# Optimization experiments

Measured on AMD Instinct MI355X. Metric: run time of the kernel, lower is better.

The kernel has to match this reference:

```python
import jax, jax.numpy as jnp
import numpy as np

B, H, W, C = 8, 128, 128, 192
G, K = 6, 3
K2 = K * K
GC = C // G
OFFSET_SCALE = 0.1
DN = ('NHWC', 'HWIO', 'NHWC')


def setup_inputs() -> dict:
    key = jax.random.key(0)
    ks = jax.random.split(key, 8)
    s = 1.0 / np.sqrt(C)
    return {
        'x': jax.random.normal(ks[0], (B, H, W, C), jnp.float32),
        'w_in': jax.random.normal(ks[1], (C, C), jnp.float32) * s,
        'b_in': jnp.zeros((C,), jnp.float32),
        'w_dw': jax.random.normal(ks[2], (3, 3, 1, C), jnp.float32) / 3.0,  # depthwise 3x3, HWIO
        'b_dw': jnp.zeros((C,), jnp.float32),
        'w_pw': jax.random.normal(ks[3], (1, 1, C, C), jnp.float32) * s,  # 1x1 conv
        'b_pw': jnp.zeros((C,), jnp.float32),
        'w_off': jax.random.normal(ks[4], (C, G * K2 * 2), jnp.float32) * 0.01,
        'b_off': jnp.zeros((G * K2 * 2,), jnp.float32),
        'w_mask': jax.random.normal(ks[5], (C, G * K2), jnp.float32) * 0.01,
        'b_mask': jnp.zeros((G * K2,), jnp.float32),
        'w_out': jax.random.normal(ks[6], (C, C), jnp.float32) * s,
        'b_out': jnp.zeros((C,), jnp.float32),
    }


def _deform_forward(x, w_in, b_in, w_dw, b_dw, w_pw, b_pw, w_off, b_off, w_mask, b_mask, w_out, b_out):
    x_proj = x @ w_in + b_in  # [B,H,W,C]

    # dw_conv: depthwise 3x3 -> SiLU -> 1x1 pointwise (all channels-last)
    xd = jax.lax.conv_general_dilated(x, w_dw, (1, 1), 'SAME', dimension_numbers=DN,
                                      feature_group_count=C) + b_dw
    xd = xd * jax.nn.sigmoid(xd)  # SiLU
    xd = jax.lax.conv_general_dilated(xd, w_pw, (1, 1), 'SAME', dimension_numbers=DN) + b_pw

    offsets = (xd @ w_off + b_off).reshape(B, H, W, G, K2, 2) * OFFSET_SCALE
    attn = jax.nn.softmax((xd @ w_mask + b_mask).reshape(B, H, W, G, K2), axis=-1)
    attn = jnp.nan_to_num(attn, nan=0.0)

    r = jnp.arange(-(K // 2), K // 2 + 1, dtype=jnp.float32)
    ref_grid = jnp.stack(jnp.meshgrid(r, r, indexing='ij'), -1).reshape(K2, 2)  # [K2,2]
    pos = ref_grid + offsets  # [B,H,W,G,K2,2]
    pos_h = jnp.clip(pos[..., 0] + jnp.arange(H, dtype=jnp.float32)[None, :, None, None, None], 0.0, H - 1)
    pos_w = jnp.clip(pos[..., 1] + jnp.arange(W, dtype=jnp.float32)[None, None, :, None, None], 0.0, W - 1)

    xg = x_proj.reshape(B, H * W, G, GC)

    def gather(hi, wi):
        idx = (hi * W + wi).reshape(B, H * W, G, 1)
        return jnp.take_along_axis(xg, idx, axis=1).reshape(B, H, W, G, GC)

    def tap(acc, inputs):
        ph, pw, a = inputs  # each [B,H,W,G]
        hf = jnp.clip(ph.astype(jnp.int32), 0, H - 1)
        wf = jnp.clip(pw.astype(jnp.int32), 0, W - 1)
        hc = jnp.minimum(hf + 1, H - 1)
        wc = jnp.minimum(wf + 1, W - 1)
        hw = ph - hf.astype(jnp.float32)
        ww = pw - wf.astype(jnp.float32)
        sampled = (gather(hf, wf) * ((1 - hw) * (1 - ww))[..., None]
                   + gather(hf, wc) * ((1 - hw) * ww)[..., None]
                   + gather(hc, wf) * (hw * (1 - ww))[..., None]
                   + gather(hc, wc) * (hw * ww)[..., None])
        return acc + sampled * a[..., None], None

    xs = (jnp.moveaxis(pos_h, -1, 0), jnp.moveaxis(pos_w, -1, 0), jnp.moveaxis(attn, -1, 0))
    out, _ = jax.lax.scan(tap, jnp.zeros((B, H, W, G, GC), x.dtype), xs)
    return out.reshape(B, H, W, C) @ w_out + b_out


def reference(x, w_in, b_in, w_dw, b_dw, w_pw, b_pw, w_off, b_off, w_mask, b_mask, w_out, b_out):
    return _deform_forward(x, w_in, b_in, w_dw, b_dw, w_pw, b_pw,
                           w_off, b_off, w_mask, b_mask, w_out, b_out)
```

## Files before the change

### kernel.cpp

```cpp
#include <hip/hip_runtime.h>
#include <hip/hip_bf16.h>

#define Bn 8
#define Hn 128
#define Wn 128
#define Cn 192
#define Gn 6
#define GCn 32
#define NPIX (Bn*Hn*Wn)

typedef __attribute__((ext_vector_type(8))) short v8s;
typedef __attribute__((ext_vector_type(4))) float v4f;
typedef __attribute__((ext_vector_type(2))) float v2f;
typedef __hip_bfloat16 bf16;

__device__ __forceinline__ float b2f(bf16 v){ return __bfloat162float(v); }
__device__ __forceinline__ float lo16(unsigned u){ return __uint_as_float(u << 16); }
__device__ __forceinline__ float hi16(unsigned u){ return __uint_as_float(u & 0xffff0000u); }
__device__ __forceinline__ v2f up2(unsigned u){
    return (v2f){ __uint_as_float(u << 16), __uint_as_float(u & 0xffff0000u) };
}

__global__ __launch_bounds__(256) void cvt_bf16(const float* __restrict__ in,
                                                bf16* __restrict__ out, long n)
{
    long base = ((long)blockIdx.x*256 + threadIdx.x)*8;
    if (base >= n) return;
    float v[8];
    *(float4*)(v)   = *(const float4*)(in + base);
    *(float4*)(v+4) = *(const float4*)(in + base + 4);
    bf16 o[8];
    #pragma unroll
    for (int j=0;j<8;j++) o[j] = __float2bfloat16(v[j]);
    *(uint4*)(out + base) = *(uint4*)o;
}

__global__ __launch_bounds__(256) void swizzle_w(const float* __restrict__ w,
                                                 bf16* __restrict__ out, int N)
{
    int idx = blockIdx.x*256 + threadIdx.x;
    int j = idx & 7, lane = (idx>>3)&63, ks = (idx>>9)%6, nt = idx/3072;
    int k = ks*32 + ((lane>>4)<<3) + j;
    int n = (nt<<4) + (lane&15);
    out[idx] = (n < N) ? __float2bfloat16(w[k*N + n]) : __float2bfloat16(0.0f);
}

__global__ __launch_bounds__(256) void swizzle_om(const float* __restrict__ woff,
        const float* __restrict__ wmask, const float* __restrict__ boff,
        const float* __restrict__ bmask, bf16* __restrict__ out, float* __restrict__ biascat)
{
    int idx = blockIdx.x*256 + threadIdx.x;
    if (idx < 192) {
        float bv = 0.0f;
        if (idx < 108) bv = boff[idx];
        else if (idx < 162) bv = bmask[idx-108];
        biascat[idx] = bv;
    }
    int j = idx & 7, lane = (idx>>3)&63, ks = (idx>>9)%6, nt = idx/3072;
    int k = ks*32 + ((lane>>4)<<3) + j;
    int n = (nt<<4) + (lane&15);
    float v = 0.0f;
    if (n < 108)      v = woff[k*108 + n];
    else if (n < 162) v = wmask[k*54 + (n-108)];
    out[idx] = __float2bfloat16(v);
}

__device__ __forceinline__ void store_out(bf16* p, float v){ *p = __float2bfloat16(v); }
__device__ __forceinline__ void store_out(float* p, float v){ *p = v; }

template<typename OutT>
__global__ __launch_bounds__(256, 2) void gemm6r(const bf16* __restrict__ A,
        const v8s* __restrict__ wfrag, const float* __restrict__ bias,
        OutT* __restrict__ Cmat, int Nreal, int Nstride)
{
    int tid = threadIdx.x;
    int wave = tid >> 6, lane = tid & 63;
    int q = lane >> 4, r = lane & 15;
    const v8s* wsrc = wfrag + blockIdx.y*(36*64) + lane;
    v8s breg[36];
    #pragma unroll
    for (int f=0; f<36; f++) breg[f] = wsrc[f*64];
    int col0 = blockIdx.y*96;
    float bv[6];
    #pragma unroll
    for (int nt=0; nt<6; nt++) {
        int col = col0 + nt*16 + r;
        bv[nt] = (col < Nreal) ? bias[col] : 0.0f;
    }
    const int MT = NPIX/64;
    for (int mt = blockIdx.x; mt < MT; mt += gridDim.x) {
        const bf16* Ap = A + (size_t)(mt*64 + wave*16 + r)*Cn + q*8;
        v8s av[6];
        #pragma unroll
        for (int ks=0; ks<6; ks++) av[ks] = *(const v8s*)(Ap + ks*32);
        v4f acc[6];
        #pragma unroll
        for (int nt=0;nt<6;nt++) acc[nt] = (v4f){0.f,0.f,0.f,0.f};
        #pragma unroll
        for (int ks=0; ks<6; ks++)
            #pragma unroll
            for (int nt=0;nt<6;nt++)
                acc[nt] = __builtin_amdgcn_mfma_f32_16x16x32_bf16(
                              av[ks], breg[nt*6+ks], acc[nt], 0, 0, 0);
        int orow = mt*64 + wave*16 + q*4;
        #pragma unroll
        for (int nt=0;nt<6;nt++) {
            int col = col0 + nt*16 + r;
            if (col < Nreal) {
                #pragma unroll
                for (int i=0;i<4;i++)
                    store_out(&Cmat[(size_t)(orow+i)*Nstride + col], acc[nt][i] + bv[nt]);
            }
        }
    }
}

__global__ __launch_bounds__(256, 4) void dw_silu(const bf16* __restrict__ x,
        const bf16* __restrict__ wdwb, const float* __restrict__ bdw, bf16* __restrict__ out)
{
    int idx = blockIdx.x*256 + threadIdx.x;
    int c16 = idx % 12; int pix = idx / 12;
    int b = pix >> 14; int hw = pix & 16383; int h = hw >> 7, w = hw & 127;
    int cb = c16*16;
    v2f acc2[8];
    #pragma unroll
    for (int j=0;j<8;j++) acc2[j] = (v2f){bdw[cb+2*j], bdw[cb+2*j+1]};
    #pragma unroll
    for (int dy=-1;dy<=1;dy++){
        int hh=h+dy; if ((unsigned)hh >= (unsigned)Hn) continue;
        #pragma unroll
        for (int dx=-1;dx<=1;dx++){
            int ww=w+dx; if ((unsigned)ww >= (unsigned)Wn) continue;
            const uint4* xp = (const uint4*)(x + ((size_t)((b<<14)+(hh<<7)+ww))*Cn + cb);
            const uint4* wp = (const uint4*)(wdwb + ((dy+1)*3+(dx+1))*Cn + cb);
            #pragma unroll
            for (int cs=0;cs<2;cs++){
                uint4 xu = xp[cs], wu = wp[cs];
                unsigned xa[4] = {xu.x,xu.y,xu.z,xu.w};
                unsigned wa[4] = {wu.x,wu.y,wu.z,wu.w};
                #pragma unroll
                for (int t=0;t<4;t++)
                    acc2[cs*4+t] += up2(xa[t]) * up2(wa[t]);
            }
        }
    }
    bf16 ov[16];
    #pragma unroll
    for (int j=0;j<8;j++){
        float v0 = acc2[j].x, v1 = acc2[j].y;
        ov[2*j]   = __float2bfloat16(v0 / (1.f + __expf(-v0)));
        ov[2*j+1] = __float2bfloat16(v1 / (1.f + __expf(-v1)));
    }
    uint4* op = (uint4*)(out + (size_t)pix*Cn + cb);
    op[0] = ((uint4*)ov)[0];
    op[1] = ((uint4*)ov)[1];
}

__global__ __launch_bounds__(256, 4) void deform_sample(const bf16* __restrict__ P,
        const bf16* __restrict__ OM, bf16* __restrict__ S)
{
    int idx = blockIdx.x*256 + threadIdx.x;
    int half = idx & 1;
    int g = (idx >> 1) % 6;
    int pix = idx / 12;
    int b = pix >> 14; int hw = pix & 16383; int h = hw >> 7, w = hw & 127;
    const bf16* om = OM + (size_t)pix*162;
    const bf16* oml = om + 108 + g*9;
    const unsigned* ofp = (const unsigned*)(om + g*18);

    float att[9];
    float m = -1e30f;
    #pragma unroll
    for (int k=0;k<9;k++){ att[k] = b2f(oml[k]); m = fmaxf(m, att[k]); }
    float ssum = 0.f;
    #pragma unroll
    for (int k=0;k<9;k++){ att[k] = __expf(att[k]-m); ssum += att[k]; }
    float inv = 1.f/ssum;

    v2f acc2[8];
    #pragma unroll
    for (int j=0;j<8;j++) acc2[j] = (v2f){0.f, 0.f};
    int chbase = g*GCn + half*16;
    const bf16* xb = P + ((((size_t)b) << 14))*Cn + chbase;
    #pragma unroll
    for (int k=0;k<9;k++){
        unsigned opair = ofp[k];
        float ph = (float)(h + k/3 - 1) + 0.1f*lo16(opair);
        float pw = (float)(w + k%3 - 1) + 0.1f*hi16(opair);
        ph = fminf(fmaxf(ph, 0.f), 127.f);
        pw = fminf(fmaxf(pw, 0.f), 127.f);
        int hf = (int)ph, wf = (int)pw;
        float fh = ph - (float)hf, fw = pw - (float)wf;
        int hc = min(hf+1,127), wc = min(wf+1,127);
        float a = att[k]*inv;
        float w00=(1.f-fh)*(1.f-fw)*a, w01=(1.f-fh)*fw*a, w10=fh*(1.f-fw)*a, w11=fh*fw*a;
        const uint4* p00 = (const uint4*)(xb + ((hf<<7)+wf)*Cn);
        const uint4* p01 = (const uint4*)(xb + ((hf<<7)+wc)*Cn);
        const uint4* p10 = (const uint4*)(xb + ((hc<<7)+wf)*Cn);
        const uint4* p11 = (const uint4*)(xb + ((hc<<7)+wc)*Cn);
        #pragma unroll
        for (int cs=0;cs<2;cs++){
            uint4 a00=p00[cs], a01=p01[cs], a10=p10[cs], a11=p11[cs];
            unsigned u00[4]={a00.x,a00.y,a00.z,a00.w};
            unsigned u01[4]={a01.x,a01.y,a01.z,a01.w};
            unsigned u10[4]={a10.x,a10.y,a10.z,a10.w};
            unsigned u11[4]={a11.x,a11.y,a11.z,a11.w};
            #pragma unroll
            for (int t=0;t<4;t++)
                acc2[cs*4+t] += up2(u00[t])*w00 + up2(u01[t])*w01
                              + up2(u10[t])*w10 + up2(u11[t])*w11;
        }
    }
    bf16 ov[16];
    #pragma unroll
    for (int j=0;j<8;j++){
        ov[2*j]   = __float2bfloat16(acc2[j].x);
        ov[2*j+1] = __float2bfloat16(acc2[j].y);
    }
    uint4* sp = (uint4*)(S + (size_t)pix*Cn + chbase);
    sp[0] = ((uint4*)ov)[0];
    sp[1] = ((uint4*)ov)[1];
}

extern "C" void kernel_launch(void* const* d_in, const int* in_sizes, int n_in,
                              void* d_out, int out_size, void* d_ws, size_t ws_size,
                              hipStream_t stream)
{
    const float* x      = (const float*)d_in[0];
    const float* w_in   = (const float*)d_in[1];
    const float* b_in   = (const float*)d_in[2];
    const float* w_dw   = (const float*)d_in[3];
    const float* b_dw   = (const float*)d_in[4];
    const float* w_pw   = (const float*)d_in[5];
    const float* b_pw   = (const float*)d_in[6];
    const float* w_off  = (const float*)d_in[7];
    const float* b_off  = (const float*)d_in[8];
    const float* w_mask = (const float*)d_in[9];
    const float* b_mask = (const float*)d_in[10];
    const float* w_out  = (const float*)d_in[11];
    const float* b_out  = (const float*)d_in[12];
    float* out = (float*)d_out;

    char* ws = (char*)d_ws;
    size_t off = 0;
    auto carve = [&](size_t bytes)->char* {
        char* p = ws + off; off += (bytes + 255) & ~(size_t)255; return p; };
    bf16* XB  = (bf16*)carve((size_t)NPIX*Cn*2);
    bf16* P   = (bf16*)carve((size_t)NPIX*Cn*2);
    bf16* D   = (bf16*)carve((size_t)NPIX*Cn*2);
    bf16* OM  = (bf16*)carve((size_t)NPIX*162*2);
    bf16* wfI = (bf16*)carve(36864*2);
    bf16* wfP = (bf16*)carve(36864*2);
    bf16* wfO = (bf16*)carve(36864*2);
    bf16* wfM = (bf16*)carve(36864*2);
    float* bM = (float*)carve(192*4);
    bf16* WDW = (bf16*)carve(1728*2);

    dim3 blk(256);
    cvt_bf16<<<12288, blk, 0, stream>>>(x, XB, (long)NPIX*Cn);
    cvt_bf16<<<1,     blk, 0, stream>>>(w_dw, WDW, 1728);
    swizzle_w<<<144, blk, 0, stream>>>(w_in,  wfI, 192);
    swizzle_w<<<144, blk, 0, stream>>>(w_pw,  wfP, 192);
    swizzle_w<<<144, blk, 0, stream>>>(w_out, wfO, 192);
    swizzle_om<<<144, blk, 0, stream>>>(w_off, w_mask, b_off, b_mask, wfM, bM);

    dim3 ggrid(512, 2);
    gemm6r<bf16><<<ggrid, blk, 0, stream>>>(XB, (const v8s*)wfI, b_in, P, 192, 192);

    dw_silu<<<6144, blk, 0, stream>>>(XB, WDW, b_dw, D);

    bf16* X2 = XB;
    gemm6r<bf16><<<ggrid, blk, 0, stream>>>(D,  (const v8s*)wfP, b_pw, X2, 192, 192);
    gemm6r<bf16><<<ggrid, blk, 0, stream>>>(X2, (const v8s*)wfM, bM,  OM, 162, 162);

    deform_sample<<<6144, blk, 0, stream>>>(P, OM, D);

    gemm6r<float><<<ggrid, blk, 0, stream>>>(D, (const v8s*)wfO, b_out, out, 192, 192);
}
```

Before: 485.6 us.

## Swizzle block IDs for XCD locality and double-buffer deform tap loads

Remaps block indices in the GEMM, depthwise and deform kernels so that consecutive logical tiles land on the same XCD (bid&7 spread). The aim is better L2 locality across the MI355X chiplets. The GEMM launch becomes a 1D grid of 1024 blocks that decodes its column half and row-tile start from the swizzled id. The deform sampler is also software-pipelined with two register buffers, so one tap's gathers are issued while the previous tap is accumulated, at the cost of more registers and possibly lower occupancy.

```diff
diff --git a/kernel.cpp b/kernel.cpp
--- a/kernel.cpp
+++ b/kernel.cpp
@@ -76,11 +76,15 @@
     int tid = threadIdx.x;
     int wave = tid >> 6, lane = tid & 63;
     int q = lane >> 4, r = lane & 15;
-    const v8s* wsrc = wfrag + blockIdx.y*(36*64) + lane;
+    int n = blockIdx.x;
+    int l = (n & 7) * 128 + (n >> 3);
+    int yhalf = l & 1;
+    int mt0 = l >> 1;
+    const v8s* wsrc = wfrag + yhalf*(36*64) + lane;
     v8s breg[36];
     #pragma unroll
     for (int f=0; f<36; f++) breg[f] = wsrc[f*64];
-    int col0 = blockIdx.y*96;
+    int col0 = yhalf*96;
     float bv[6];
     #pragma unroll
     for (int nt=0; nt<6; nt++) {
@@ -88,7 +92,7 @@
         bv[nt] = (col < Nreal) ? bias[col] : 0.0f;
     }
     const int MT = NPIX/64;
-    for (int mt = blockIdx.x; mt < MT; mt += gridDim.x) {
+    for (int mt = mt0; mt < MT; mt += 512) {
         const bf16* Ap = A + (size_t)(mt*64 + wave*16 + r)*Cn + q*8;
         v8s av[6];
         #pragma unroll
@@ -118,7 +122,9 @@
 __global__ __launch_bounds__(256, 4) void dw_silu(const bf16* __restrict__ x,
         const bf16* __restrict__ wdwb, const float* __restrict__ bdw, bf16* __restrict__ out)
 {
-    int idx = blockIdx.x*256 + threadIdx.x;
+    int bid = blockIdx.x;
+    int bsw = (bid & 7) * 768 + (bid >> 3);
+    int idx = bsw*256 + threadIdx.x;
     int c16 = idx % 12; int pix = idx / 12;
     int b = pix >> 14; int hw = pix & 16383; int h = hw >> 7, w = hw & 127;
     int cb = c16*16;
@@ -156,10 +162,43 @@
     op[1] = ((uint4*)ov)[1];
 }
 
+
+#define LOADTAP(K, S)                                                        \
+  { float ph = (float)(h + (K)/3 - 1) + 0.1f*lo16(op[K]);                    \
+    float pw = (float)(w + (K)%3 - 1) + 0.1f*hi16(op[K]);                    \
+    ph = fminf(fmaxf(ph, 0.f), 127.f);                                       \
+    pw = fminf(fmaxf(pw, 0.f), 127.f);                                       \
+    int hf = (int)ph, wf = (int)pw;                                          \
+    fh##S = ph - (float)hf; fw##S = pw - (float)wf;                          \
+    int hc = min(hf+1,127), wc = min(wf+1,127);                              \
+    const uint4* p00 = (const uint4*)(xb + ((hf<<7)+wf)*Cn);                 \
+    const uint4* p01 = (const uint4*)(xb + ((hf<<7)+wc)*Cn);                 \
+    const uint4* p10 = (const uint4*)(xb + ((hc<<7)+wf)*Cn);                 \
+    const uint4* p11 = (const uint4*)(xb + ((hc<<7)+wc)*Cn);                 \
+    S##00[0]=p00[0]; S##00[1]=p00[1]; S##01[0]=p01[0]; S##01[1]=p01[1];      \
+    S##10[0]=p10[0]; S##10[1]=p10[1]; S##11[0]=p11[0]; S##11[1]=p11[1]; }
+
+#define ACCTAP(K, S)                                                         \
+  { float a = att[K];                                                        \
+    float w00=(1.f-fh##S)*(1.f-fw##S)*a, w01=(1.f-fh##S)*fw##S*a,            \
+          w10=fh##S*(1.f-fw##S)*a, w11=fh##S*fw##S*a;                        \
+    _Pragma("unroll")                                                        \
+    for (int cs=0;cs<2;cs++){                                                \
+      unsigned u00[4]={S##00[cs].x,S##00[cs].y,S##00[cs].z,S##00[cs].w};     \
+      unsigned u01[4]={S##01[cs].x,S##01[cs].y,S##01[cs].z,S##01[cs].w};     \
+      unsigned u10[4]={S##10[cs].x,S##10[cs].y,S##10[cs].z,S##10[cs].w};     \
+      unsigned u11[4]={S##11[cs].x,S##11[cs].y,S##11[cs].z,S##11[cs].w};     \
+      _Pragma("unroll")                                                      \
+      for (int t=0;t<4;t++)                                                  \
+        acc2[cs*4+t] += up2(u00[t])*w00 + up2(u01[t])*w01                    \
+                      + up2(u10[t])*w10 + up2(u11[t])*w11; } }
+
 __global__ __launch_bounds__(256, 4) void deform_sample(const bf16* __restrict__ P,
         const bf16* __restrict__ OM, bf16* __restrict__ S)
 {
-    int idx = blockIdx.x*256 + threadIdx.x;
+    int bid = blockIdx.x;
+    int bsw = (bid & 7) * 768 + (bid >> 3);
+    int idx = bsw*256 + threadIdx.x;
     int half = idx & 1;
     int g = (idx >> 1) % 6;
     int pix = idx / 12;
@@ -168,6 +207,10 @@
     const bf16* oml = om + 108 + g*9;
     const unsigned* ofp = (const unsigned*)(om + g*18);
 
+    unsigned op[9];
+    #pragma unroll
+    for (int k=0;k<9;k++) op[k] = ofp[k];
+
     float att[9];
     float m = -1e30f;
     #pragma unroll
@@ -176,41 +219,31 @@
     #pragma unroll
     for (int k=0;k<9;k++){ att[k] = __expf(att[k]-m); ssum += att[k]; }
     float inv = 1.f/ssum;
-
-    v2f acc2[8];
-    #pragma unroll
-    for (int j=0;j<8;j++) acc2[j] = (v2f){0.f, 0.f};
+    #pragma unroll
+    for (int k=0;k<9;k++) att[k] *= inv;
+
     int chbase = g*GCn + half*16;
     const bf16* xb = P + ((((size_t)b) << 14))*Cn + chbase;
-    #pragma unroll
-    for (int k=0;k<9;k++){
-        unsigned opair = ofp[k];
-        float ph = (float)(h + k/3 - 1) + 0.1f*lo16(opair);
-        float pw = (float)(w + k%3 - 1) + 0.1f*hi16(opair);
-        ph = fminf(fmaxf(ph, 0.f), 127.f);
-        pw = fminf(fmaxf(pw, 0.f), 127.f);
-        int hf = (int)ph, wf = (int)pw;
-        float fh = ph - (float)hf, fw = pw - (float)wf;
-        int hc = min(hf+1,127), wc = min(wf+1,127);
-        float a = att[k]*inv;
-        float w00=(1.f-fh)*(1.f-fw)*a, w01=(1.f-fh)*fw*a, w10=fh*(1.f-fw)*a, w11=fh*fw*a;
-        const uint4* p00 = (const uint4*)(xb + ((hf<<7)+wf)*Cn);
-        const uint4* p01 = (const uint4*)(xb + ((hf<<7)+wc)*Cn);
-        const uint4* p10 = (const uint4*)(xb + ((hc<<7)+wf)*Cn);
-        const uint4* p11 = (const uint4*)(xb + ((hc<<7)+wc)*Cn);
-        #pragma unroll
-        for (int cs=0;cs<2;cs++){
-            uint4 a00=p00[cs], a01=p01[cs], a10=p10[cs], a11=p11[cs];
-            unsigned u00[4]={a00.x,a00.y,a00.z,a00.w};
-            unsigned u01[4]={a01.x,a01.y,a01.z,a01.w};
-            unsigned u10[4]={a10.x,a10.y,a10.z,a10.w};
-            unsigned u11[4]={a11.x,a11.y,a11.z,a11.w};
-            #pragma unroll
-            for (int t=0;t<4;t++)
-                acc2[cs*4+t] += up2(u00[t])*w00 + up2(u01[t])*w01
-                              + up2(u10[t])*w10 + up2(u11[t])*w11;
-        }
-    }
+
+    v2f acc2[8];
+    #pragma unroll
+    for (int j=0;j<8;j++) acc2[j] = (v2f){0.f, 0.f};
+
+    uint4 A00[2],A01[2],A10[2],A11[2]; float fhA,fwA;
+    uint4 B00[2],B01[2],B10[2],B11[2]; float fhB,fwB;
+
+    LOADTAP(0, A)
+    LOADTAP(1, B)
+    ACCTAP(0, A)  LOADTAP(2, A)
+    ACCTAP(1, B)  LOADTAP(3, B)
+    ACCTAP(2, A)  LOADTAP(4, A)
+    ACCTAP(3, B)  LOADTAP(5, B)
+    ACCTAP(4, A)  LOADTAP(6, A)
+    ACCTAP(5, B)  LOADTAP(7, B)
+    ACCTAP(6, A)  LOADTAP(8, A)
+    ACCTAP(7, B)
+    ACCTAP(8, A)
+
     bf16 ov[16];
     #pragma unroll
     for (int j=0;j<8;j++){
@@ -264,16 +297,15 @@
     swizzle_w<<<144, blk, 0, stream>>>(w_out, wfO, 192);
     swizzle_om<<<144, blk, 0, stream>>>(w_off, w_mask, b_off, b_mask, wfM, bM);
 
-    dim3 ggrid(512, 2);
-    gemm6r<bf16><<<ggrid, blk, 0, stream>>>(XB, (const v8s*)wfI, b_in, P, 192, 192);
+    gemm6r<bf16><<<1024, blk, 0, stream>>>(XB, (const v8s*)wfI, b_in, P, 192, 192);
 
     dw_silu<<<6144, blk, 0, stream>>>(XB, WDW, b_dw, D);
 
     bf16* X2 = XB;
-    gemm6r<bf16><<<ggrid, blk, 0, stream>>>(D,  (const v8s*)wfP, b_pw, X2, 192, 192);
-    gemm6r<bf16><<<ggrid, blk, 0, stream>>>(X2, (const v8s*)wfM, bM,  OM, 162, 162);
+    gemm6r<bf16><<<1024, blk, 0, stream>>>(D,  (const v8s*)wfP, b_pw, X2, 192, 192);
+    gemm6r<bf16><<<1024, blk, 0, stream>>>(X2, (const v8s*)wfM, bM,  OM, 162, 162);
 
     deform_sample<<<6144, blk, 0, stream>>>(P, OM, D);
 
-    gemm6r<float><<<ggrid, blk, 0, stream>>>(D, (const v8s*)wfO, b_out, out, 192, 192);
-}
+    gemm6r<float><<<1024, blk, 0, stream>>>(D, (const v8s*)wfO, b_out, out, 192, 192);
+}
```

Result: faster. 418.9 us (-13.7%).
